# Optimization experiments

Hardware: AMD Instinct MI355X
Metric: run time of the kernel (lower is better)

## Reference

```python
import jax, jax.numpy as jnp
import numpy as np

GROUPSIZE = 128
IN_F, OUT_F = 4096, 11008
TOKENS = 512


def setup_inputs() -> dict:
    key = jax.random.key(0)
    k1, k2, k3, k4, k5 = jax.random.split(key, 5)
    x = jax.random.normal(k1, (TOKENS, IN_F), dtype=jnp.float32)
    # packed 4-bit codes: two nibbles per byte, stored as int32 in [0, 256)
    qweight = jax.random.randint(k2, (OUT_F * IN_F // 2,), 0, 256, dtype=jnp.int32)
    n_groups = OUT_F * IN_F // GROUPSIZE
    scales = jax.random.uniform(k3, (n_groups, 1), dtype=jnp.float32) * 0.02 + 1e-3
    zeros = jax.random.uniform(k4, (n_groups, 1), dtype=jnp.float32) * 15.0
    bias = jax.random.normal(k5, (OUT_F,), dtype=jnp.float32)
    return {"x": x, "qweight": qweight, "scales": scales, "zeros": zeros, "bias": bias}


def _dequant_w4(qweight, scales, zeros, dtype):
    # python_decompress: high nibble then low nibble, each in [0,16)
    hi = (qweight >> 4) % 16
    lo = qweight % 16
    codes = jnp.stack([hi, lo], axis=-1).reshape(-1, GROUPSIZE).astype(dtype)
    # group-wise dequant: (code - zero) * scale, zeros/scales are (n_groups, 1)
    w = (codes - zeros.astype(dtype)) * scales.astype(dtype)
    return w.reshape(OUT_F, IN_F)


def reference(x, qweight, scales, zeros, bias):
    w = _dequant_w4(qweight, scales, zeros, x.dtype)  # [out, in]
    return x @ w.T + bias
```

## Files before the change

kernel.cpp:

```cpp
#include <hip/hip_runtime.h>

#define GROUPSIZE 128
#define IN_F 4096
#define OUT_F 11008
#define TOKENS 512
#define N_GROUPS (OUT_F * IN_F / GROUPSIZE)

#define BM 64
#define BN 128
#define BK 64
#define NTHREADS 256
#define NT (IN_F / BK)

typedef _Float16 half8  __attribute__((ext_vector_type(8)));
typedef _Float16 half2v __attribute__((ext_vector_type(2)));
typedef float    f32x4  __attribute__((ext_vector_type(4)));
typedef int      ivec4  __attribute__((ext_vector_type(4)));

__device__ __forceinline__ int swz(int r, int k) {
    return ((r << 6) + k) ^ ((r & 7) << 3);
}

__device__ __forceinline__ void glds16(const _Float16* g, _Float16* l) {
    __builtin_amdgcn_global_load_lds(
        (const __attribute__((address_space(1))) void*)g,
        (__attribute__((address_space(3))) void*)l, 16, 0, 0);
}

__global__ __launch_bounds__(256)
void cvt_x_kernel(const float* __restrict__ x, _Float16* __restrict__ x16) {
    size_t i = ((size_t)blockIdx.x * 256 + threadIdx.x) * 8;
    f32x4 a = *(const f32x4*)(x + i);
    f32x4 b = *(const f32x4*)(x + i + 4);
    half8 h;
    h[0]=(_Float16)a[0]; h[1]=(_Float16)a[1]; h[2]=(_Float16)a[2]; h[3]=(_Float16)a[3];
    h[4]=(_Float16)b[0]; h[5]=(_Float16)b[1]; h[6]=(_Float16)b[2]; h[7]=(_Float16)b[3];
    *(half8*)(x16 + i) = h;
}

__global__ __launch_bounds__(256)
void szpack_kernel(const float* __restrict__ s, const float* __restrict__ z,
                   uint2* __restrict__ szp) {
    int g = blockIdx.x * 256 + threadIdx.x;
    if (g >= N_GROUPS) return;
    _Float16 S = (_Float16)s[g];
    _Float16 B = (_Float16)(-(64.0f + z[g]) * (float)S);
    unsigned short su = __builtin_bit_cast(unsigned short, S);
    unsigned short bu = __builtin_bit_cast(unsigned short, B);
    uint2 r;
    r.x = ((unsigned)su << 16) | su;
    r.y = ((unsigned)bu << 16) | bu;
    szp[g] = r;
}

__device__ __forceinline__ half8 dq8(ivec4 q, uint2 sz) {
    half2v S  = __builtin_bit_cast(half2v, sz.x);
    half2v Bv = __builtin_bit_cast(half2v, sz.y);
    half8 r;
#pragma unroll
    for (int e = 0; e < 4; ++e) {
        unsigned qq = (unsigned)q[e];
        unsigned u = ((qq & 0xF0u) | ((qq << 20) & 0x00F00000u)) | 0x54005400u;
        half2v h = __builtin_bit_cast(half2v, u);
        half2v w = h * S + Bv;
        r[2*e]   = w[0];
        r[2*e+1] = w[1];
    }
    return r;
}

__global__ __launch_bounds__(NTHREADS, 3)
void qlinear_main(const _Float16* __restrict__ x16,
                  const int*   __restrict__ qw,
                  const uint2* __restrict__ szp,
                  const float* __restrict__ bias,
                  float*       __restrict__ out)
{
    __shared__ __align__(16) _Float16 As[2][BM * BK];
    __shared__ __align__(16) _Float16 Bs[2][BN * BK];

    const int tid = threadIdx.x;
    const int m0 = blockIdx.x * BM;
    const int n0 = blockIdx.y * BN;
    const int wv = tid >> 6, ln = tid & 63;

    const int s8 = tid & 7;
    const int r0 = tid >> 3;
    const int* qg = qw + (size_t)(n0 + r0) * (IN_F / 2) + s8 * 4;
    const int szb = (n0 + r0) * (IN_F / GROUPSIZE);

    const int ar  = wv * 16 + (ln >> 3);
    const int gsw = (ln & 7) ^ ((ln >> 3) & 7);
    const _Float16* ag = x16 + (size_t)(m0 + ar) * IN_F + gsw * 8;

    const int wr = (wv >> 1) * 32, wc = (wv & 1) * 64;
    const int lr = ln & 15, lk8 = (ln >> 4) * 8, lk4 = (ln >> 4) * 4;

    f32x4 acc[2][4];
#pragma unroll
    for (int i = 0; i < 2; ++i)
#pragma unroll
        for (int j = 0; j < 4; ++j)
            acc[i][j] = (f32x4){0.f, 0.f, 0.f, 0.f};

#define LOAD_Q(qs, szs, tt) do {                                            \
        _Pragma("unroll")                                                   \
        for (int j = 0; j < 4; ++j) {                                       \
            qs[j]  = *(const ivec4*)(qg + (size_t)j * 32 * (IN_F/2) + (tt) * 32); \
            szs[j] = szp[szb + j * 32 * (IN_F/GROUPSIZE) + ((tt) >> 1)];    \
        }                                                                   \
    } while (0)

#define STAGE_A(tt, buf) do {                                      \
        const _Float16* gp = ag + (size_t)(tt) * 64;               \
        glds16(gp,             &As[buf][wv * 1024]);               \
        glds16(gp + 8 * IN_F,  &As[buf][wv * 1024 + 512]);         \
    } while (0)

#define DQ_STORE(qs, szs, buf) do {                                        \
        _Pragma("unroll")                                                  \
        for (int j = 0; j < 4; ++j)                                        \
            *(half8*)&Bs[buf][swz(r0 + 32 * j, s8 * 8)] = dq8(qs[j], szs[j]); \
    } while (0)

    auto mfma_phase = [&](int buf) {
#pragma unroll
        for (int kk = 0; kk < 2; ++kk) {
            half8 af[2], bf[4];
#pragma unroll
            for (int i = 0; i < 2; ++i)
                af[i] = *(const half8*)&As[buf][swz(wr + i * 16 + lr, kk * 32 + lk8)];
#pragma unroll
            for (int j = 0; j < 4; ++j)
                bf[j] = *(const half8*)&Bs[buf][swz(wc + j * 16 + lr, kk * 32 + lk8)];
#pragma unroll
            for (int i = 0; i < 2; ++i)
#pragma unroll
                for (int j = 0; j < 4; ++j)
                    acc[i][j] = __builtin_amdgcn_mfma_f32_16x16x32_f16(
                        af[i], bf[j], acc[i][j], 0, 0, 0);
        }
    };

    ivec4 qA[4], qB[4];
    uint2 szA[4], szB[4];
    LOAD_Q(qA, szA, 0);
    LOAD_Q(qB, szB, 1);
    STAGE_A(0, 0);
    DQ_STORE(qA, szA, 0);
    __syncthreads();

    for (int t = 0; t < NT; t += 2) {
        {
            const int tl = (t + 2 < NT) ? t + 2 : NT - 1;
            LOAD_Q(qA, szA, tl);
            STAGE_A((t + 1 < NT) ? t + 1 : NT - 1, 1);
            DQ_STORE(qB, szB, 1);
            mfma_phase(0);
            __syncthreads();
        }
        {
            const int tl = (t + 3 < NT) ? t + 3 : NT - 1;
            LOAD_Q(qB, szB, tl);
            STAGE_A((t + 2 < NT) ? t + 2 : NT - 1, 0);
            DQ_STORE(qA, szA, 0);
            mfma_phase(1);
            __syncthreads();
        }
    }

#pragma unroll
    for (int j = 0; j < 4; ++j) {
        const int col = n0 + wc + j * 16 + lr;
        const float bv = bias[col];
#pragma unroll
        for (int i = 0; i < 2; ++i) {
            const int rb = m0 + wr + i * 16 + lk4;
#pragma unroll
            for (int r = 0; r < 4; ++r)
                out[(size_t)(rb + r) * OUT_F + col] = acc[i][j][r] + bv;
        }
    }
#undef LOAD_Q
#undef STAGE_A
#undef DQ_STORE
}

extern "C" void kernel_launch(void* const* d_in, const int* in_sizes, int n_in,
                              void* d_out, int out_size, void* d_ws, size_t ws_size,
                              hipStream_t stream) {
    const float* x      = (const float*)d_in[0];
    const int*   qw     = (const int*)d_in[1];
    const float* scales = (const float*)d_in[2];
    const float* zeros  = (const float*)d_in[3];
    const float* bias   = (const float*)d_in[4];
    float*       out    = (float*)d_out;

    _Float16* x16 = (_Float16*)d_ws;
    uint2*    szp = (uint2*)((char*)d_ws + (size_t)TOKENS * IN_F * 2);

    cvt_x_kernel<<<TOKENS * IN_F / (256 * 8), 256, 0, stream>>>(x, x16);
    szpack_kernel<<<(N_GROUPS + 255) / 256, 256, 0, stream>>>(scales, zeros, szp);

    dim3 grid(TOKENS / BM, OUT_F / BN);
    qlinear_main<<<grid, NTHREADS, 0, stream>>>(x16, qw, szp, bias, out);
}
```

Before: 255.0 us.

## Remap blocks per XCD for weight reuse and relax barrier waits to partial vmcnt

The launch becomes a 1D grid of 704 blocks. Each XCD (chosen by bid&7) gets a contiguous range of N tiles, and the M tiles sit innermost, so blocks sharing the same quantized weight tile land on the same XCD's L2. The __syncthreads calls become an explicit s_waitcnt vmcnt(8) lgkmcnt(0) plus barrier. The A staging is issued before the Q loads, so the barrier waits only for the older A LDS copies and leaves the prefetched weight loads in flight. This relies on the vmcnt count matching the number of outstanding loads. If the compiler reorders memory ops, that could become a correctness risk.

```diff
diff --git a/kernel.cpp b/kernel.cpp
--- a/kernel.cpp
+++ b/kernel.cpp
@@ -11,6 +11,7 @@
 #define BK 64
 #define NTHREADS 256
 #define NT (IN_F / BK)
+#define NTILES_N (OUT_F / BN)
 
 typedef _Float16 half8  __attribute__((ext_vector_type(8)));
 typedef _Float16 half2v __attribute__((ext_vector_type(2)));
@@ -26,6 +27,11 @@
         (const __attribute__((address_space(1))) void*)g,
         (__attribute__((address_space(3))) void*)l, 16, 0, 0);
 }
+
+#define WAITBAR8() do {                                                  \
+        asm volatile("s_waitcnt vmcnt(8) lgkmcnt(0)" ::: "memory");      \
+        __builtin_amdgcn_s_barrier();                                    \
+    } while (0)
 
 __global__ __launch_bounds__(256)
 void cvt_x_kernel(const float* __restrict__ x, _Float16* __restrict__ x16) {
@@ -79,9 +85,16 @@
     __shared__ __align__(16) _Float16 As[2][BM * BK];
     __shared__ __align__(16) _Float16 Bs[2][BN * BK];
 
+    const int bid = blockIdx.x;
+    const int xcd = bid & 7;
+    const int s   = bid >> 3;
+    const int n_t = 11 * xcd + (s >> 3);
+    const int m_t = s & 7;
+    if (n_t >= NTILES_N) return;
+    const int n0 = n_t * BN;
+    const int m0 = m_t * BM;
+
     const int tid = threadIdx.x;
-    const int m0 = blockIdx.x * BM;
-    const int n0 = blockIdx.y * BN;
     const int wv = tid >> 6, ln = tid & 63;
 
     const int s8 = tid & 7;
@@ -145,27 +158,29 @@
     ivec4 qA[4], qB[4];
     uint2 szA[4], szB[4];
     LOAD_Q(qA, szA, 0);
+    STAGE_A(0, 0);
     LOAD_Q(qB, szB, 1);
-    STAGE_A(0, 0);
     DQ_STORE(qA, szA, 0);
-    __syncthreads();
+    WAITBAR8();
 
     for (int t = 0; t < NT; t += 2) {
         {
-            const int tl = (t + 2 < NT) ? t + 2 : NT - 1;
-            LOAD_Q(qA, szA, tl);
-            STAGE_A((t + 1 < NT) ? t + 1 : NT - 1, 1);
+            const int ta = (t + 1 < NT) ? t + 1 : NT - 1;
+            const int tq = (t + 2 < NT) ? t + 2 : NT - 1;
+            STAGE_A(ta, 1);
+            LOAD_Q(qA, szA, tq);
             DQ_STORE(qB, szB, 1);
             mfma_phase(0);
-            __syncthreads();
+            WAITBAR8();
         }
         {
-            const int tl = (t + 3 < NT) ? t + 3 : NT - 1;
-            LOAD_Q(qB, szB, tl);
-            STAGE_A((t + 2 < NT) ? t + 2 : NT - 1, 0);
+            const int ta = (t + 2 < NT) ? t + 2 : NT - 1;
+            const int tq = (t + 3 < NT) ? t + 3 : NT - 1;
+            STAGE_A(ta, 0);
+            LOAD_Q(qB, szB, tq);
             DQ_STORE(qA, szA, 0);
             mfma_phase(1);
-            __syncthreads();
+            WAITBAR8();
         }
     }
 
@@ -202,6 +217,5 @@
     cvt_x_kernel<<<TOKENS * IN_F / (256 * 8), 256, 0, stream>>>(x, x16);
     szpack_kernel<<<(N_GROUPS + 255) / 256, 256, 0, stream>>>(scales, zeros, szp);
 
-    dim3 grid(TOKENS / BM, OUT_F / BN);
-    qlinear_main<<<grid, NTHREADS, 0, stream>>>(x16, qw, szp, bias, out);
-}
+    qlinear_main<<<704, NTHREADS, 0, stream>>>(x16, qw, szp, bias, out);
+}
```

Measured after the change: 252.1 us. No clear change (-1.2%).
